# Kernel optimization log

Hardware: AMD Instinct MI355X
Metric: run time of the kernel (lower is better)

The kernel has to match this reference:

```python
import jax, jax.numpy as jnp
import numpy as np

BN_EPS = 1e-5


def _gin_layer(h, src, dst, w1, b1, w2, b2, gamma, beta):
    n = h.shape[0]
    # GINConv, eps=0: MLP(x + sum_{j->i} x_j); messages gathered at src, scattered to dst
    agg = jax.ops.segment_sum(h[src], dst, num_segments=n)
    h = agg + h
    h = jnp.maximum(h @ w1 + b1, 0.0) @ w2 + b2
    h = jnp.maximum(h, 0.0)  # F.relu after conv
    # BatchNorm1d, training-mode batch statistics (biased var)
    mean = h.mean(axis=0)
    var = h.var(axis=0)
    return (h - mean) * jax.lax.rsqrt(var + BN_EPS) * gamma + beta


def setup_inputs() -> dict:
    key = jax.random.key(0)
    ks = jax.random.split(key, 32)
    N, E, F_IN, DIM, L, G = 100000, 1600000, 128, 64, 3, 1000
    inp = {
        "x": jax.random.normal(ks[0], (N, F_IN), dtype=jnp.float32),
        "edge_index": jax.random.randint(ks[1], (2, E), 0, N, dtype=jnp.int64),
        "batch": jnp.sort(jax.random.randint(ks[2], (N,), 0, G, dtype=jnp.int64)),
        "num_graphs": G,
    }
    k = 3
    for i in range(L):
        din = F_IN if i == 0 else DIM
        inp[f"l{i}_w1"] = jax.random.normal(ks[k], (din, DIM), dtype=jnp.float32) * 0.05; k += 1
        inp[f"l{i}_b1"] = jnp.zeros((DIM,), dtype=jnp.float32)
        inp[f"l{i}_w2"] = jax.random.normal(ks[k], (DIM, DIM), dtype=jnp.float32) * 0.05; k += 1
        inp[f"l{i}_b2"] = jnp.zeros((DIM,), dtype=jnp.float32)
        inp[f"l{i}_gamma"] = jnp.ones((DIM,), dtype=jnp.float32)
        inp[f"l{i}_beta"] = jnp.zeros((DIM,), dtype=jnp.float32)
    return inp


def reference(x, edge_index, batch, num_graphs,
              l0_w1, l0_b1, l0_w2, l0_b2, l0_gamma, l0_beta,
              l1_w1, l1_b1, l1_w2, l1_b2, l1_gamma, l1_beta,
              l2_w1, l2_b1, l2_w2, l2_b2, l2_gamma, l2_beta):
    src, dst = edge_index[0], edge_index[1]
    params = [
        (l0_w1, l0_b1, l0_w2, l0_b2, l0_gamma, l0_beta),
        (l1_w1, l1_b1, l1_w2, l1_b2, l1_gamma, l1_beta),
        (l2_w1, l2_b1, l2_w2, l2_b2, l2_gamma, l2_beta),
    ]
    h = x
    xs = []
    for p in params:
        h = _gin_layer(h, src, dst, *p)
        xs.append(h)
    # global_add_pool per layer, then concat along features
    xpool = [jax.ops.segment_sum(h, batch, num_segments=num_graphs) for h in xs]
    return jnp.concatenate(xpool, axis=1), jnp.concatenate(xs, axis=1)
```

## Files before the change

### kernel.cpp

```cpp
#include <hip/hip_runtime.h>

#define DIM 64
#define XS_STRIDE 192
#define BN_EPS 1e-5f
#define B_MAX 512
#define P4_CAP 6144
#define CSR_CHUNK 16384
#define BSPACE 1280

__device__ inline unsigned pack_bf16x2(float lo, float hi) {
    unsigned ulo = __float_as_uint(lo); ulo = (ulo + 0x7FFFu + ((ulo >> 16) & 1u)) >> 16;
    unsigned uhi = __float_as_uint(hi); uhi = (uhi + 0x7FFFu + ((uhi >> 16) & 1u)) >> 16;
    return ulo | (uhi << 16);
}
__device__ inline float2 unpack_bf16x2(unsigned v) {
    return make_float2(__uint_as_float(v << 16), __uint_as_float(v & 0xFFFF0000u));
}

__global__ __launch_bounds__(256) void p1_hist(const int* __restrict__ dsts, long long E,
                                               int NB1, int B, int* __restrict__ bh,
                                               float* __restrict__ stats,
                                               unsigned* __restrict__ ybf, int N) {
    __shared__ int hist[B_MAX];
    const int i = blockIdx.x, t = threadIdx.x;
    if (i == 0) {
        for (int k = t; k < 3 * 256; k += 256) stats[k] = 0.f;
        if (t < 32) ybf[(size_t)N * 32 + t] = 0u;
    }
    for (int b = t; b < B; b += 256) hist[b] = 0;
    __syncthreads();
    long long s0 = (long long)i * CSR_CHUNK;
    long long s1 = s0 + CSR_CHUNK; if (s1 > E) s1 = E;
    for (long long e = s0 + t; e < s1; e += 256)
        atomicAdd(&hist[dsts[e] >> 8], 1);
    __syncthreads();
    for (int b = t; b < B; b += 256) bh[b * NB1 + i] = hist[b];
}

__global__ __launch_bounds__(1024) void p2_scan(int* __restrict__ bh, int total_n) {
    __shared__ int sbuf[2][1024];
    const int t = threadIdx.x;
    const int seg = (total_n + 1023) / 1024;
    int s0 = t * seg, s1 = s0 + seg; if (s1 > total_n) s1 = total_n;
    int s = 0;
    for (int i = s0; i < s1; i++) s += bh[i];
    sbuf[0][t] = s; __syncthreads();
    int c = 0;
    for (int o = 1; o < 1024; o <<= 1) {
        int val = sbuf[c][t];
        if (t >= o) val += sbuf[c][t - o];
        sbuf[c ^ 1][t] = val; __syncthreads(); c ^= 1;
    }
    int run = sbuf[c][t] - s;
    for (int i = s0; i < s1; i++) { int v = bh[i]; bh[i] = run; run += v; }
}

__global__ __launch_bounds__(256) void p3proj_kernel(
    const int* __restrict__ edges, long long E, int NB1, int B,
    const int* __restrict__ bh, unsigned* __restrict__ ebuf,
    const float* __restrict__ x, int F_IN,
    const float* __restrict__ w1, unsigned* __restrict__ ybf, int N)
{
    __shared__ int cur[B_MAX];
    __shared__ float w1s[128 * DIM];
    __shared__ float hin[32][128];
    const int t = threadIdx.x;

    if (blockIdx.x < NB1) {
        const int i = blockIdx.x;
        for (int b = t; b < B; b += 256) cur[b] = bh[b * NB1 + i];
        __syncthreads();
        long long s0 = (long long)i * CSR_CHUNK;
        long long s1 = s0 + CSR_CHUNK; if (s1 > E) s1 = E;
        for (long long e = s0 + t; e < s1; e += 256) {
            int src = edges[e];
            int dst = edges[E + e];
            int b = dst >> 8;
            int pos = atomicAdd(&cur[b], 1);
            ebuf[pos] = (unsigned)src | ((unsigned)(dst & 255) << 24);
        }
        return;
    }
    const int row0 = (blockIdx.x - NB1) * 32;
    for (int i = t; i < 128 * DIM / 4; i += 256)
        *(float4*)&w1s[i * 4] = *(const float4*)&w1[i * 4];
    for (int i = t; i < 32 * 128 / 4; i += 256) {
        int r = i / 32, k4 = (i % 32) * 4;
        int row = row0 + r;
        float4 hv = make_float4(0.f, 0.f, 0.f, 0.f);
        if (row < N) hv = *(const float4*)&x[(size_t)row * F_IN + k4];
        *(float4*)&hin[r][k4] = hv;
    }
    __syncthreads();

    const int hw = t >> 5;
    const int hl = t & 31;
    float a0[4], a1[4];
    #pragma unroll
    for (int q = 0; q < 4; q++) { a0[q] = 0.f; a1[q] = 0.f; }
    for (int k = 0; k < 128; k++) {
        float w0 = w1s[k * DIM + 2 * hl];
        float w1v = w1s[k * DIM + 2 * hl + 1];
        #pragma unroll
        for (int q = 0; q < 4; q++) {
            float hv = hin[hw * 4 + q][k];
            a0[q] += hv * w0; a1[q] += hv * w1v;
        }
    }
    #pragma unroll
    for (int q = 0; q < 4; q++) {
        int row = row0 + hw * 4 + q;
        if (row < N) ybf[(size_t)row * 32 + hl] = pack_bf16x2(a0[q], a1[q]);
    }
}

__global__ __launch_bounds__(256) void p4_build(const unsigned* __restrict__ ebuf, long long E,
                                                int NB1, int B, const int* __restrict__ bh,
                                                int* __restrict__ offsets, int* __restrict__ psz,
                                                int* __restrict__ eidx, int N) {
    __shared__ unsigned lbuf[P4_CAP];
    __shared__ int hist[256];
    __shared__ int sbuf[2][256];
    __shared__ int cur[256];
    __shared__ int lstart[256];
    const int b = blockIdx.x, t = threadIdx.x;
    const int s = bh[b * NB1];
    const int e = (b + 1 < B) ? bh[(b + 1) * NB1] : (int)E;
    const int sz = e - s;
    const int ps = ((s + 3) & ~3) + b * BSPACE;
    const int next_raw = (b + 1 < B) ? bh[(b + 1) * NB1] : (int)E;
    const int next_ps = ((next_raw + 3) & ~3) + (b + 1) * BSPACE;
    const bool inl = (sz <= P4_CAP);
    if (inl) for (int k = t; k < sz; k += 256) lbuf[k] = ebuf[s + k];
    hist[t] = 0;
    __syncthreads();
    for (int k = t; k < sz; k += 256) {
        unsigned v = inl ? lbuf[k] : ebuf[s + k];
        atomicAdd(&hist[v >> 24], 1);
    }
    __syncthreads();
    const int deg = hist[t];
    const int pad = max(4, (deg + 3) & ~3);
    sbuf[0][t] = pad; __syncthreads();
    int c = 0;
    for (int o = 1; o < 256; o <<= 1) {
        int val = sbuf[c][t];
        if (t >= o) val += sbuf[c][t - o];
        sbuf[c ^ 1][t] = val; __syncthreads(); c ^= 1;
    }
    const int excl = sbuf[c][t] - pad;
    const int total = sbuf[c][255];
    const int node = b * 256 + t;
    if (node < N) { offsets[node] = ps + excl; psz[node] = pad; }
    lstart[t] = excl;
    cur[t] = 0;
    __syncthreads();
    for (int k = t; k < sz; k += 256) {
        unsigned v = inl ? lbuf[k] : ebuf[s + k];
        int dl = v >> 24;
        int pos = atomicAdd(&cur[dl], 1);
        eidx[ps + lstart[dl] + pos] = (int)(v & 0xFFFFFFu);
    }
    for (int k = deg; k < pad; k++) eidx[ps + excl + k] = N;
    __syncthreads();
    for (int i = ps + total + t; i < next_ps; i += 256) eidx[i] = N;
}

template<int DIN, bool FUSE>
__global__ __launch_bounds__(256) void proj_kernel(
    const float* __restrict__ h, int h_stride, int h_off,
    float* __restrict__ h_back,
    const float* __restrict__ w1,
    const float* __restrict__ stats_prev,
    const float* __restrict__ gamma_prev, const float* __restrict__ beta_prev,
    unsigned* __restrict__ ybf, int N)
{
    constexpr int R = 32;
    __shared__ float w1s[DIN * DIM];
    __shared__ float hin[R][DIN];
    __shared__ float scshs[2 * DIM];
    const int tid = threadIdx.x;
    const int row0 = blockIdx.x * R;

    if (FUSE && tid < DIM) {
        float inv_n = 1.0f / (float)N;
        float mean = stats_prev[tid] * inv_n;
        float var  = stats_prev[DIM + tid] * inv_n - mean * mean;
        float sc   = gamma_prev[tid] * rsqrtf(var + BN_EPS);
        scshs[tid] = sc;
        scshs[DIM + tid] = beta_prev[tid] - mean * sc;
    }
    for (int i = tid; i < DIN * DIM / 4; i += 256)
        *(float4*)&w1s[i * 4] = *(const float4*)&w1[i * 4];
    if (FUSE) __syncthreads();
    for (int i = tid; i < R * DIN / 4; i += 256) {
        int r = i / (DIN / 4), k4 = (i % (DIN / 4)) * 4;
        int row = row0 + r;
        float4 hv = make_float4(0.f, 0.f, 0.f, 0.f);
        if (row < N) {
            hv = *(const float4*)&h[(size_t)row * h_stride + h_off + k4];
            if (FUSE) {
                hv.x = hv.x * scshs[k4 + 0] + scshs[DIM + k4 + 0];
                hv.y = hv.y * scshs[k4 + 1] + scshs[DIM + k4 + 1];
                hv.z = hv.z * scshs[k4 + 2] + scshs[DIM + k4 + 2];
                hv.w = hv.w * scshs[k4 + 3] + scshs[DIM + k4 + 3];
                *(float4*)&h_back[(size_t)row * h_stride + h_off + k4] = hv;
            }
        }
        *(float4*)&hin[r][k4] = hv;
    }
    __syncthreads();

    const int hw = tid >> 5;
    const int hl = tid & 31;
    float a0[4], a1[4];
    #pragma unroll
    for (int q = 0; q < 4; q++) { a0[q] = 0.f; a1[q] = 0.f; }
    for (int k = 0; k < DIN; k++) {
        float w0 = w1s[k * DIM + 2 * hl];
        float w1v = w1s[k * DIM + 2 * hl + 1];
        #pragma unroll
        for (int q = 0; q < 4; q++) {
            float hv = hin[hw * 4 + q][k];
            a0[q] += hv * w0; a1[q] += hv * w1v;
        }
    }
    #pragma unroll
    for (int q = 0; q < 4; q++) {
        int row = row0 + hw * 4 + q;
        if (row < N) ybf[(size_t)row * 32 + hl] = pack_bf16x2(a0[q], a1[q]);
    }
}

template<bool WITH_POOL>
__global__ __launch_bounds__(256) void aggmlp_kernel(
    const unsigned* __restrict__ ybf,
    const int* __restrict__ offsets, const int* __restrict__ psz,
    const int* __restrict__ eidx,
    const float* __restrict__ b1,
    const float* __restrict__ w2, const float* __restrict__ b2,
    float* __restrict__ xs, int xs_off,
    float* __restrict__ stats, int N,
    int ablocks, const int* __restrict__ batch, float* __restrict__ pool)
{
    constexpr int R = 64;
    __shared__ float zin[R][DIM];
    __shared__ float sred[2][DIM];
    const int tid  = threadIdx.x;

    if (WITH_POOL && blockIdx.x >= ablocks) {
        const int g = blockIdx.x - ablocks;
        const int half = tid >> 7, c = tid & 127;
        int lo = 0, hi = N;
        while (lo < hi) { int mid = (lo + hi) >> 1; if (batch[mid] < g) lo = mid + 1; else hi = mid; }
        int start = lo;
        hi = N;
        while (lo < hi) { int mid = (lo + hi) >> 1; if (batch[mid] < g + 1) lo = mid + 1; else hi = mid; }
        int end = lo;
        int mid2 = (start + end) >> 1;
        int rs = half ? mid2 : start;
        int re = half ? end : mid2;
        float s = 0.f;
        for (int n = rs; n < re; n++) s += xs[(size_t)n * XS_STRIDE + c];
        sred[half][c & 63] = 0.f;
        zin[half][c & 63] = 0.f;
        __syncthreads();
        __shared__ float psum[2][128];
        psum[half][c] = s;
        __syncthreads();
        if (half == 0) pool[(size_t)g * XS_STRIDE + c] = psum[0][c] + psum[1][c];
        return;
    }

    const int row0 = blockIdx.x * R;
    const int qw = tid >> 4;
    const int ql = tid & 15;
    const uint2* __restrict__ ybf2 = (const uint2*)ybf;

    if (tid < DIM) { sred[0][tid] = 0.f; sred[1][tid] = 0.f; }

    const float4 b1v = *(const float4*)&b1[ql * 4];
    int p0[4], sz[4];
    float ac[4][4];
    #pragma unroll
    for (int q = 0; q < 4; q++) {
        int node = row0 + qw * 4 + q;
        if (node < N) {
            p0[q] = offsets[node];
            sz[q] = psz[node];
            uint2 sv = ybf2[(size_t)node * 16 + ql];
            float2 lo = unpack_bf16x2(sv.x), hi = unpack_bf16x2(sv.y);
            ac[q][0] = lo.x + b1v.x; ac[q][1] = lo.y + b1v.y;
            ac[q][2] = hi.x + b1v.z; ac[q][3] = hi.y + b1v.w;
        } else {
            p0[q] = 0; sz[q] = 0;
            ac[q][0] = ac[q][1] = ac[q][2] = ac[q][3] = 0.f;
        }
    }
    int steps = 0;
    #pragma unroll
    for (int q = 0; q < 4; q++) steps = max(steps, sz[q] >> 2);

    int4 e4[4];
    #pragma unroll
    for (int q = 0; q < 4; q++)
        e4[q] = *(const int4*)&eidx[p0[q]];

    for (int s = 0; s < steps; s++) {
        const int b4 = 4 * s;
        uint2 g[4][4];
        #pragma unroll
        for (int q = 0; q < 4; q++) {
            g[q][0] = ybf2[(size_t)e4[q].x * 16 + ql];
            g[q][1] = ybf2[(size_t)e4[q].y * 16 + ql];
            g[q][2] = ybf2[(size_t)e4[q].z * 16 + ql];
            g[q][3] = ybf2[(size_t)e4[q].w * 16 + ql];
        }
        int4 e4n[4];
        #pragma unroll
        for (int q = 0; q < 4; q++) {
            int off = max(0, min(b4 + 4, sz[q] - 4));
            e4n[q] = *(const int4*)&eidx[p0[q] + off];
        }
        #pragma unroll
        for (int q = 0; q < 4; q++) {
            const float m = (b4 < sz[q]) ? 1.f : 0.f;
            #pragma unroll
            for (int j = 0; j < 4; j++) {
                float2 lo = unpack_bf16x2(g[q][j].x), hi = unpack_bf16x2(g[q][j].y);
                ac[q][0] += lo.x * m; ac[q][1] += lo.y * m;
                ac[q][2] += hi.x * m; ac[q][3] += hi.y * m;
            }
        }
        #pragma unroll
        for (int q = 0; q < 4; q++) e4[q] = e4n[q];
    }
    #pragma unroll
    for (int q = 0; q < 4; q++) {
        int r = qw * 4 + q;
        float4 z;
        z.x = fmaxf(ac[q][0], 0.f); z.y = fmaxf(ac[q][1], 0.f);
        z.z = fmaxf(ac[q][2], 0.f); z.w = fmaxf(ac[q][3], 0.f);
        *(float4*)&zin[r][ql * 4] = z;
    }
    __syncthreads();

    const int lane = tid & 63;
    const int wv_  = tid >> 6;
    float oacc[16];
    #pragma unroll
    for (int i = 0; i < 16; i++) oacc[i] = b2[lane];
    for (int k = 0; k < DIM; k++) {
        float w = w2[k * DIM + lane];
        #pragma unroll
        for (int i = 0; i < 16; i++) oacc[i] += zin[wv_ + 4 * i][k] * w;
    }
    float s1 = 0.f, s2 = 0.f;
    #pragma unroll
    for (int i = 0; i < 16; i++) {
        int row = row0 + wv_ + 4 * i;
        if (row < N) {
            float v = fmaxf(oacc[i], 0.f);
            xs[(size_t)row * XS_STRIDE + xs_off + lane] = v;
            s1 += v; s2 += v * v;
        }
    }
    atomicAdd(&sred[0][lane], s1);
    atomicAdd(&sred[1][lane], s2);
    __syncthreads();
    if (tid < DIM) {
        atomicAdd(&stats[tid], sred[0][tid]);
        atomicAdd(&stats[DIM + tid], sred[1][tid]);
    }
}

__global__ void poolB_kernel(float* __restrict__ xs, const int* __restrict__ batch,
                             float* __restrict__ pool,
                             const float* __restrict__ stats2,
                             const float* __restrict__ gamma2, const float* __restrict__ beta2,
                             int N) {
    int g = blockIdx.x;
    int c = threadIdx.x;
    float inv_n = 1.0f / (float)N;
    float mean = stats2[c] * inv_n;
    float var  = stats2[DIM + c] * inv_n - mean * mean;
    float sc = gamma2[c] * rsqrtf(var + BN_EPS);
    float sh = beta2[c] - mean * sc;
    int lo = 0, hi = N;
    while (lo < hi) { int mid = (lo + hi) >> 1; if (batch[mid] < g) lo = mid + 1; else hi = mid; }
    int start = lo;
    hi = N;
    while (lo < hi) { int mid = (lo + hi) >> 1; if (batch[mid] < g + 1) lo = mid + 1; else hi = mid; }
    int end = lo;
    float s = 0.f;
    for (int n = start; n < end; n++) {
        size_t p = (size_t)n * XS_STRIDE + 2 * DIM + c;
        float v = xs[p] * sc + sh;
        xs[p] = v;
        s += v;
    }
    pool[(size_t)g * XS_STRIDE + 2 * DIM + c] = s;
}

extern "C" void kernel_launch(void* const* d_in, const int* in_sizes, int n_in,
                              void* d_out, int out_size, void* d_ws, size_t ws_size,
                              hipStream_t stream) {
    const float* x     = (const float*)d_in[0];
    const int*   edges = (const int*)d_in[1];
    const int*   batch = (const int*)d_in[2];

    const int  N    = in_sizes[2];
    const long long E = in_sizes[1] / 2;
    const int  F_IN = in_sizes[0] / N;
    const int  G    = out_size / XS_STRIDE - N;

    const float* W[3][6];
    for (int l = 0; l < 3; l++)
        for (int p = 0; p < 6; p++)
            W[l][p] = (const float*)d_in[4 + l * 6 + p];

    float* out_pool = (float*)d_out;
    float* out_xs   = out_pool + (size_t)G * XS_STRIDE;

    const int B   = (N + 255) >> 8;
    const int NB1 = (int)((E + CSR_CHUNK - 1) / CSR_CHUNK);
    const int EPAD = (int)(((E + 3) & ~3LL) + (long long)B * BSPACE + 64);

    unsigned* ybf  = (unsigned*)d_ws;
    float* stats   = (float*)(ybf + (size_t)(N + 1) * 32);
    int*   offsets = (int*)(stats + 3 * 256);
    int*   psz     = offsets + N + 1;
    int*   eidx    = psz + N;
    unsigned* ebuf = (unsigned*)(eidx + EPAD);
    int*   bh      = (int*)(ebuf + E);

    const int pblocks = (N + 31) / 32;
    const int ablocks = (N + 63) / 64;

    p1_hist<<<NB1, 256, 0, stream>>>(edges + E, E, NB1, B, bh, stats, ybf, N);
    p2_scan<<<1, 1024, 0, stream>>>(bh, B * NB1);
    p3proj_kernel<<<NB1 + pblocks, 256, 0, stream>>>(edges, E, NB1, B, bh, ebuf,
                                                     x, F_IN, W[0][0], ybf, N);
    p4_build<<<B, 256, 0, stream>>>(ebuf, E, NB1, B, bh, offsets, psz, eidx, N);

    aggmlp_kernel<false><<<ablocks, 256, 0, stream>>>(ybf, offsets, psz, eidx,
        W[0][1], W[0][2], W[0][3], out_xs, 0, stats, N, ablocks, nullptr, nullptr);

    proj_kernel<64, true><<<pblocks, 256, 0, stream>>>(
        out_xs, XS_STRIDE, 0, out_xs, W[1][0], stats, W[0][4], W[0][5], ybf, N);
    aggmlp_kernel<false><<<ablocks, 256, 0, stream>>>(ybf, offsets, psz, eidx,
        W[1][1], W[1][2], W[1][3], out_xs, DIM, stats + 256, N, ablocks, nullptr, nullptr);

    proj_kernel<64, true><<<pblocks, 256, 0, stream>>>(
        out_xs, XS_STRIDE, DIM, out_xs, W[2][0], stats + 256, W[1][4], W[1][5], ybf, N);
    aggmlp_kernel<true><<<ablocks + G, 256, 0, stream>>>(ybf, offsets, psz, eidx,
        W[2][1], W[2][2], W[2][3], out_xs, 2 * DIM, stats + 512, N, ablocks, batch, out_pool);

    poolB_kernel<<<G, DIM, 0, stream>>>(out_xs, batch, out_pool,
                                        stats + 512, W[2][4], W[2][5], N);
}
```

Measured before the change: 434.5 us.

## Move layer-0 projection into histogram kernel and halve CSR chunk size

The first-layer X·W1 projection blocks now ride along with the destination histogram pass instead of the partition pass, so the partition kernel runs alone. The histogram loop gets an int4 vectorized fast path for full chunks, and CSR_CHUNK is halved to launch more histogram and partition blocks. Halving the chunk doubles NB1, which makes the bucket-histogram table larger and lengthens the serial scan. A redundant shared-memory zeroing and barrier is also dropped from the pooling branch.

Measured after the change: 498.0 us. 14.6% more time.

```diff
diff --git a/kernel.cpp b/kernel.cpp
--- a/kernel.cpp
+++ b/kernel.cpp
@@ -5,7 +5,7 @@
 #define BN_EPS 1e-5f
 #define B_MAX 512
 #define P4_CAP 6144
-#define CSR_CHUNK 16384
+#define CSR_CHUNK 8192
 #define BSPACE 1280
 
 __device__ inline unsigned pack_bf16x2(float lo, float hi) {
@@ -17,24 +17,76 @@
     return make_float2(__uint_as_float(v << 16), __uint_as_float(v & 0xFFFF0000u));
 }
 
-__global__ __launch_bounds__(256) void p1_hist(const int* __restrict__ dsts, long long E,
-                                               int NB1, int B, int* __restrict__ bh,
-                                               float* __restrict__ stats,
-                                               unsigned* __restrict__ ybf, int N) {
+__global__ __launch_bounds__(256) void p1proj_kernel(
+    const int* __restrict__ dsts, long long E, int NB1, int B, int* __restrict__ bh,
+    float* __restrict__ stats,
+    const float* __restrict__ x, int F_IN,
+    const float* __restrict__ w1, unsigned* __restrict__ ybf, int N)
+{
     __shared__ int hist[B_MAX];
-    const int i = blockIdx.x, t = threadIdx.x;
-    if (i == 0) {
-        for (int k = t; k < 3 * 256; k += 256) stats[k] = 0.f;
-        if (t < 32) ybf[(size_t)N * 32 + t] = 0u;
-    }
-    for (int b = t; b < B; b += 256) hist[b] = 0;
-    __syncthreads();
-    long long s0 = (long long)i * CSR_CHUNK;
-    long long s1 = s0 + CSR_CHUNK; if (s1 > E) s1 = E;
-    for (long long e = s0 + t; e < s1; e += 256)
-        atomicAdd(&hist[dsts[e] >> 8], 1);
-    __syncthreads();
-    for (int b = t; b < B; b += 256) bh[b * NB1 + i] = hist[b];
+    __shared__ float w1s[128 * DIM];
+    __shared__ float hin[32][128];
+    const int t = threadIdx.x;
+
+    if (blockIdx.x < NB1) {
+        const int i = blockIdx.x;
+        if (i == 0) {
+            for (int k = t; k < 3 * 256; k += 256) stats[k] = 0.f;
+            if (t < 32) ybf[(size_t)N * 32 + t] = 0u;
+        }
+        for (int b = t; b < B; b += 256) hist[b] = 0;
+        __syncthreads();
+        long long s0 = (long long)i * CSR_CHUNK;
+        long long s1 = s0 + CSR_CHUNK; if (s1 > E) s1 = E;
+        if (s1 - s0 == CSR_CHUNK) {
+            const int4* d4 = (const int4*)(dsts + s0);
+            #pragma unroll
+            for (int k = 0; k < CSR_CHUNK / 1024; k++) {
+                int4 v = d4[k * 256 + t];
+                atomicAdd(&hist[v.x >> 8], 1);
+                atomicAdd(&hist[v.y >> 8], 1);
+                atomicAdd(&hist[v.z >> 8], 1);
+                atomicAdd(&hist[v.w >> 8], 1);
+            }
+        } else {
+            for (long long e = s0 + t; e < s1; e += 256)
+                atomicAdd(&hist[dsts[e] >> 8], 1);
+        }
+        __syncthreads();
+        for (int b = t; b < B; b += 256) bh[b * NB1 + i] = hist[b];
+        return;
+    }
+    const int row0 = (blockIdx.x - NB1) * 32;
+    for (int i = t; i < 128 * DIM / 4; i += 256)
+        *(float4*)&w1s[i * 4] = *(const float4*)&w1[i * 4];
+    for (int i = t; i < 32 * 128 / 4; i += 256) {
+        int r = i / 32, k4 = (i % 32) * 4;
+        int row = row0 + r;
+        float4 hv = make_float4(0.f, 0.f, 0.f, 0.f);
+        if (row < N) hv = *(const float4*)&x[(size_t)row * F_IN + k4];
+        *(float4*)&hin[r][k4] = hv;
+    }
+    __syncthreads();
+
+    const int hw = t >> 5;
+    const int hl = t & 31;
+    float a0[4], a1[4];
+    #pragma unroll
+    for (int q = 0; q < 4; q++) { a0[q] = 0.f; a1[q] = 0.f; }
+    for (int k = 0; k < 128; k++) {
+        float w0 = w1s[k * DIM + 2 * hl];
+        float w1v = w1s[k * DIM + 2 * hl + 1];
+        #pragma unroll
+        for (int q = 0; q < 4; q++) {
+            float hv = hin[hw * 4 + q][k];
+            a0[q] += hv * w0; a1[q] += hv * w1v;
+        }
+    }
+    #pragma unroll
+    for (int q = 0; q < 4; q++) {
+        int row = row0 + hw * 4 + q;
+        if (row < N) ybf[(size_t)row * 32 + hl] = pack_bf16x2(a0[q], a1[q]);
+    }
 }
 
 __global__ __launch_bounds__(1024) void p2_scan(int* __restrict__ bh, int total_n) {
@@ -55,62 +107,21 @@
     for (int i = s0; i < s1; i++) { int v = bh[i]; bh[i] = run; run += v; }
 }
 
-__global__ __launch_bounds__(256) void p3proj_kernel(
-    const int* __restrict__ edges, long long E, int NB1, int B,
-    const int* __restrict__ bh, unsigned* __restrict__ ebuf,
-    const float* __restrict__ x, int F_IN,
-    const float* __restrict__ w1, unsigned* __restrict__ ybf, int N)
-{
+__global__ __launch_bounds__(256) void p3_part(const int* __restrict__ edges, long long E,
+                                               int NB1, int B, const int* __restrict__ bh,
+                                               unsigned* __restrict__ ebuf) {
     __shared__ int cur[B_MAX];
-    __shared__ float w1s[128 * DIM];
-    __shared__ float hin[32][128];
-    const int t = threadIdx.x;
-
-    if (blockIdx.x < NB1) {
-        const int i = blockIdx.x;
-        for (int b = t; b < B; b += 256) cur[b] = bh[b * NB1 + i];
-        __syncthreads();
-        long long s0 = (long long)i * CSR_CHUNK;
-        long long s1 = s0 + CSR_CHUNK; if (s1 > E) s1 = E;
-        for (long long e = s0 + t; e < s1; e += 256) {
-            int src = edges[e];
-            int dst = edges[E + e];
-            int b = dst >> 8;
-            int pos = atomicAdd(&cur[b], 1);
-            ebuf[pos] = (unsigned)src | ((unsigned)(dst & 255) << 24);
-        }
-        return;
-    }
-    const int row0 = (blockIdx.x - NB1) * 32;
-    for (int i = t; i < 128 * DIM / 4; i += 256)
-        *(float4*)&w1s[i * 4] = *(const float4*)&w1[i * 4];
-    for (int i = t; i < 32 * 128 / 4; i += 256) {
-        int r = i / 32, k4 = (i % 32) * 4;
-        int row = row0 + r;
-        float4 hv = make_float4(0.f, 0.f, 0.f, 0.f);
-        if (row < N) hv = *(const float4*)&x[(size_t)row * F_IN + k4];
-        *(float4*)&hin[r][k4] = hv;
-    }
-    __syncthreads();
-
-    const int hw = t >> 5;
-    const int hl = t & 31;
-    float a0[4], a1[4];
-    #pragma unroll
-    for (int q = 0; q < 4; q++) { a0[q] = 0.f; a1[q] = 0.f; }
-    for (int k = 0; k < 128; k++) {
-        float w0 = w1s[k * DIM + 2 * hl];
-        float w1v = w1s[k * DIM + 2 * hl + 1];
-        #pragma unroll
-        for (int q = 0; q < 4; q++) {
-            float hv = hin[hw * 4 + q][k];
-            a0[q] += hv * w0; a1[q] += hv * w1v;
-        }
-    }
-    #pragma unroll
-    for (int q = 0; q < 4; q++) {
-        int row = row0 + hw * 4 + q;
-        if (row < N) ybf[(size_t)row * 32 + hl] = pack_bf16x2(a0[q], a1[q]);
+    const int i = blockIdx.x, t = threadIdx.x;
+    for (int b = t; b < B; b += 256) cur[b] = bh[b * NB1 + i];
+    __syncthreads();
+    long long s0 = (long long)i * CSR_CHUNK;
+    long long s1 = s0 + CSR_CHUNK; if (s1 > E) s1 = E;
+    for (long long e = s0 + t; e < s1; e += 256) {
+        int src = edges[e];
+        int dst = edges[E + e];
+        int b = dst >> 8;
+        int pos = atomicAdd(&cur[b], 1);
+        ebuf[pos] = (unsigned)src | ((unsigned)(dst & 255) << 24);
     }
 }
 
@@ -262,9 +273,6 @@
         int re = half ? end : mid2;
         float s = 0.f;
         for (int n = rs; n < re; n++) s += xs[(size_t)n * XS_STRIDE + c];
-        sred[half][c & 63] = 0.f;
-        zin[half][c & 63] = 0.f;
-        __syncthreads();
         __shared__ float psum[2][128];
         psum[half][c] = s;
         __syncthreads();
@@ -437,10 +445,10 @@
     const int pblocks = (N + 31) / 32;
     const int ablocks = (N + 63) / 64;
 
-    p1_hist<<<NB1, 256, 0, stream>>>(edges + E, E, NB1, B, bh, stats, ybf, N);
+    p1proj_kernel<<<NB1 + pblocks, 256, 0, stream>>>(edges + E, E, NB1, B, bh, stats,
+                                                     x, F_IN, W[0][0], ybf, N);
     p2_scan<<<1, 1024, 0, stream>>>(bh, B * NB1);
-    p3proj_kernel<<<NB1 + pblocks, 256, 0, stream>>>(edges, E, NB1, B, bh, ebuf,
-                                                     x, F_IN, W[0][0], ybf, N);
+    p3_part<<<NB1, 256, 0, stream>>>(edges, E, NB1, B, bh, ebuf);
     p4_build<<<B, 256, 0, stream>>>(ebuf, E, NB1, B, bh, offsets, psz, eidx, N);
 
     aggmlp_kernel<false><<<ablocks, 256, 0, stream>>>(ybf, offsets, psz, eidx,
```
